# Kernel optimization log

Measured on AMD Instinct MI355X. Metric: run time of the kernel, lower is better.

The kernel has to match this reference:

```python
import jax, jax.numpy as jnp
import numpy as np

N_HEAD = 16


def setup_inputs() -> dict:
    key = jax.random.key(0)
    ks = jax.random.split(key, 5)
    B, T, C = 4, 2048, 1024
    # torch Linear stored as [out,in]; we use [in,out] so x @ W matches x @ W_t.T
    return {
        "x": jax.random.normal(ks[0], (B, T, C), jnp.float32),
        "c_attn_w": jax.random.normal(ks[1], (C, 3 * C), jnp.float32) * 0.02,
        "c_attn_b": jax.random.normal(ks[2], (3 * C,), jnp.float32) * 0.02,
        "c_proj_w": jax.random.normal(ks[3], (C, C), jnp.float32) * 0.02,
        "c_proj_b": jax.random.normal(ks[4], (C,), jnp.float32) * 0.02,
    }


def reference(x, c_attn_w, c_attn_b, c_proj_w, c_proj_b):
    B, T, C = x.shape
    H = N_HEAD
    d = C // H
    qkv = x @ c_attn_w + c_attn_b                      # [B,T,3C]
    q, k, v = jnp.split(qkv, 3, axis=2)
    q = q.reshape(B, T, H, d).transpose(0, 2, 1, 3)    # [B,H,T,d]
    k = k.reshape(B, T, H, d).transpose(0, 2, 1, 3)
    v = v.reshape(B, T, H, d).transpose(0, 2, 1, 3)
    scale = 1.0 / jnp.sqrt(jnp.asarray(d, x.dtype))
    w = jnp.einsum("bhqd,bhkd->bhqk", q, k) * scale    # [B,H,T,T]
    causal = jnp.tril(jnp.ones((T, T), bool))
    w = jnp.where(causal, w, jnp.asarray(-jnp.inf, w.dtype))
    w = jax.nn.softmax(w, axis=-1)
    y = jnp.einsum("bhqk,bhkd->bhqd", w, v)            # [B,H,T,d]
    y = y.transpose(0, 2, 1, 3).reshape(B, T, C)
    return y @ c_proj_w + c_proj_b
```

## Files before the change

kernel.cpp:

```cpp
#include <hip/hip_runtime.h>
#include <hip/hip_bf16.h>
#include <stdint.h>

#define DEV __device__ __forceinline__

typedef __attribute__((ext_vector_type(8))) short short8;
typedef __attribute__((ext_vector_type(8))) _Float16 half8;
typedef __attribute__((ext_vector_type(2))) __fp16 fp16x2;
typedef __attribute__((ext_vector_type(4))) float floatx4;
typedef __attribute__((ext_vector_type(16))) float floatx16;

DEV unsigned short f2bf(float f) {
  union { float f; uint32_t u; } v; v.f = f;
  uint32_t u = v.u;
  u += 0x7fffu + ((u >> 16) & 1u);
  return (unsigned short)(u >> 16);
}
DEV unsigned short f2h(float f) {
  union { _Float16 h; unsigned short u; } c; c.h = (_Float16)f; return c.u;
}
DEV void async_cp16(const unsigned short* g, unsigned short* l) {
  __builtin_amdgcn_global_load_lds(
      (const __attribute__((address_space(1))) uint32_t*)g,
      (__attribute__((address_space(3))) uint32_t*)l, 16, 0, 0);
}

__global__ __launch_bounds__(256)
void cvt_x_kernel(const float* __restrict__ x, unsigned short* __restrict__ xb) {
  const size_t i = ((size_t)blockIdx.x * 256 + threadIdx.x) * 4;
  const float4 f = *(const float4*)(x + i);
  ushort4 w;
  w.x = f2bf(f.x); w.y = f2bf(f.y); w.z = f2bf(f.z); w.w = f2bf(f.w);
  *(ushort4*)(xb + i) = w;
}

__global__ __launch_bounds__(256)
void transpose_w_kernel(const float* __restrict__ W, unsigned short* __restrict__ Wt,
                        int K, int N) {
  __shared__ float tile[64][65];
  const int k0 = blockIdx.y * 64, n0 = blockIdx.x * 64;
  const int tr = threadIdx.x >> 4;
  const int tc = (threadIdx.x & 15) * 4;
#pragma unroll
  for (int it = 0; it < 4; ++it) {
    const int k = tr + it * 16;
    const float4 f = *(const float4*)(W + (size_t)(k0 + k) * N + n0 + tc);
    tile[k][tc + 0] = f.x; tile[k][tc + 1] = f.y;
    tile[k][tc + 2] = f.z; tile[k][tc + 3] = f.w;
  }
  __syncthreads();
#pragma unroll
  for (int it = 0; it < 4; ++it) {
    const int n = tr + it * 16;
    ushort4 w;
    w.x = f2bf(tile[tc + 0][n]); w.y = f2bf(tile[tc + 1][n]);
    w.z = f2bf(tile[tc + 2][n]); w.w = f2bf(tile[tc + 3][n]);
    *(ushort4*)(Wt + (size_t)(n0 + n) * K + k0 + tc) = w;
  }
}

template <int EPI>
__global__ __launch_bounds__(256)
void gemm_bt_kernel(const unsigned short* __restrict__ A,
                    const unsigned short* __restrict__ Bt,
                    const float* __restrict__ bias, int M, int N, int K,
                    unsigned short* __restrict__ qws,
                    unsigned short* __restrict__ kws,
                    unsigned short* __restrict__ vws,
                    float* __restrict__ out) {
  __shared__ __align__(16) unsigned short As[128 * 32];
  __shared__ __align__(16) unsigned short Bs[128 * 32];
  const int tid = threadIdx.x;
  const int wid = tid >> 6, lane = tid & 63;
  const int quad = lane >> 4, l16 = lane & 15;
  const int wm = wid >> 1, wn = wid & 1;
  const int rowA0 = blockIdx.y * 128;
  const int colB0 = blockIdx.x * 128;

  const int srow = wid * 32 + (lane >> 2);
  const int sko = (lane & 3) * 8;
  const unsigned short* gA0 = A + (size_t)(rowA0 + srow) * K + sko;
  const unsigned short* gA1 = A + (size_t)(rowA0 + srow + 16) * K + sko;
  const unsigned short* gB0 = Bt + (size_t)(colB0 + srow) * K + sko;
  const unsigned short* gB1 = Bt + (size_t)(colB0 + srow + 16) * K + sko;
  unsigned short* lA0 = &As[(wid * 128 + 0) * 8];
  unsigned short* lA1 = &As[(wid * 128 + 64) * 8];
  unsigned short* lB0 = &Bs[(wid * 128 + 0) * 8];
  unsigned short* lB1 = &Bs[(wid * 128 + 64) * 8];

  floatx4 acc[4][4];
#pragma unroll
  for (int i = 0; i < 4; ++i)
#pragma unroll
    for (int j = 0; j < 4; ++j) acc[i][j] = (floatx4){0.f, 0.f, 0.f, 0.f};

  for (int kt = 0; kt < K; kt += 32) {
    __syncthreads();
    async_cp16(gA0 + kt, lA0);
    async_cp16(gA1 + kt, lA1);
    async_cp16(gB0 + kt, lB0);
    async_cp16(gB1 + kt, lB1);
    __syncthreads();

    short8 af[4], bfr[4];
#pragma unroll
    for (int i = 0; i < 4; ++i) {
      af[i] = *(const short8*)&As[(wm * 64 + i * 16 + l16) * 32 + quad * 8];
      bfr[i] = *(const short8*)&Bs[(wn * 64 + i * 16 + l16) * 32 + quad * 8];
    }
#pragma unroll
    for (int i = 0; i < 4; ++i)
#pragma unroll
      for (int j = 0; j < 4; ++j)
        acc[i][j] =
            __builtin_amdgcn_mfma_f32_16x16x32_bf16(af[i], bfr[j], acc[i][j], 0, 0, 0);
  }

#pragma unroll
  for (int i = 0; i < 4; ++i) {
#pragma unroll
    for (int j = 0; j < 4; ++j) {
      const int row0 = rowA0 + wm * 64 + i * 16 + quad * 4;
      const int col = colB0 + wn * 64 + j * 16 + l16;
      const float bv = bias[col];
#pragma unroll
      for (int r = 0; r < 4; ++r) {
        const float v = acc[i][j][r] + bv;
        const int R = row0 + r;
        if constexpr (EPI == 0) {
          const int b = R >> 11, t = R & 2047;
          const int which = col >> 10, c = col & 1023;
          const int h = c >> 6, dd = c & 63;
          const size_t bh = (size_t)(b * 16 + h);
          if (which == 0)
            qws[(bh * 2048 + t) * 64 + dd] = f2bf(v * 0.125f);
          else if (which == 1)
            kws[(bh * 2048 + t) * 64 + dd] = f2bf(v);
          else
            vws[(bh * 64 + dd) * 2048 + t] = f2h(v);
        } else {
          out[(size_t)R * N + col] = v;
        }
      }
    }
  }
}

__global__ __launch_bounds__(256, 2)
void attn_mfma_kernel(const unsigned short* __restrict__ qws,
                      const unsigned short* __restrict__ kws,
                      const unsigned short* __restrict__ vws,
                      unsigned short* __restrict__ yws) {
  constexpr int T = 2048, D = 64;
  __shared__ __align__(16) unsigned short Ks[128 * 72];
  __shared__ __align__(16) unsigned short Vs[64 * 136];
  const int tid = threadIdx.x;
  const int wid = tid >> 6, lane = tid & 63;
  const int hf = lane >> 5, l32 = lane & 31;
  const int bh = blockIdx.x;
  const int qt = 15 - (int)blockIdx.y;
  const int qbase = qt * 128;
  const unsigned short* Qp = qws + (size_t)bh * T * D;
  const unsigned short* Kp = kws + (size_t)bh * T * D;
  const unsigned short* Vp = vws + (size_t)bh * D * T;

  const int q = qbase + wid * 32 + l32;
  short8 qf[4];
#pragma unroll
  for (int s = 0; s < 4; ++s)
    qf[s] = *(const short8*)(Qp + (size_t)q * D + s * 16 + hf * 8);

  floatx16 Oacc[2];
#pragma unroll
  for (int mt2 = 0; mt2 < 2; ++mt2)
#pragma unroll
    for (int i = 0; i < 16; ++i) Oacc[mt2][i] = 0.f;
  float mrun = -1e30f, lrun = 0.f;

  for (int kt = 0; kt <= qt; ++kt) {
    const int kb = kt * 128;
    __syncthreads();
#pragma unroll
    for (int it = 0; it < 4; ++it) {
      const int e = it * 256 + tid;
      {
        const int row = e >> 3, c = (e & 7) * 8;
        *(short8*)&Ks[row * 72 + c] =
            *(const short8*)(Kp + (size_t)(kb + row) * D + c);
      }
      {
        const int row = e >> 4, c = (e & 15) * 8;
        *(short8*)&Vs[row * 136 + c] =
            *(const short8*)(Vp + (size_t)row * T + kb + c);
      }
    }
    __syncthreads();

    const bool diag = (kt == qt);
    const int mtmax = diag ? (wid + 1) : 4;

    floatx16 S[4];
#pragma unroll
    for (int mt = 0; mt < 4; ++mt)
      if (mt < mtmax)
#pragma unroll
        for (int i = 0; i < 16; ++i) S[mt][i] = 0.f;

#pragma unroll
    for (int s = 0; s < 4; ++s) {
#pragma unroll
      for (int mt = 0; mt < 4; ++mt)
        if (mt < mtmax) {
          const short8 kf =
              *(const short8*)&Ks[(mt * 32 + l32) * 72 + s * 16 + hf * 8];
          S[mt] = __builtin_amdgcn_mfma_f32_32x32x16_bf16(kf, qf[s], S[mt], 0, 0, 0);
        }
    }

    if (diag) {
#pragma unroll
      for (int mt = 0; mt < 4; ++mt)
        if (mt == wid) {
#pragma unroll
          for (int r = 0; r < 16; ++r) {
            const int intra = (r & 3) + 8 * (r >> 2) + 4 * hf;
            if (intra > l32) S[mt][r] = -1e30f;
          }
        }
    }

    float tmax = -1e30f;
#pragma unroll
    for (int mt = 0; mt < 4; ++mt)
      if (mt < mtmax)
#pragma unroll
        for (int r = 0; r < 16; ++r) tmax = fmaxf(tmax, S[mt][r]);
    tmax = fmaxf(tmax, __shfl_xor(tmax, 32, 64));
    const float mn = fmaxf(mrun, tmax);
    const float alpha = __expf(mrun - mn);
    mrun = mn;

    float tsum = 0.f;
    uint32_t pk[4][8];
#pragma unroll
    for (int mt = 0; mt < 4; ++mt)
      if (mt < mtmax)
#pragma unroll
        for (int t = 0; t < 8; ++t) {
          const float pa = __expf(S[mt][2 * t] - mn);
          const float pb = __expf(S[mt][2 * t + 1] - mn);
          tsum += pa + pb;
          union { fp16x2 h; uint32_t u; } cv;
          cv.h = __builtin_amdgcn_cvt_pkrtz(pa, pb);
          pk[mt][t] = cv.u;
        }
    tsum += __shfl_xor(tsum, 32, 64);
    lrun = lrun * alpha + tsum;
#pragma unroll
    for (int mt2 = 0; mt2 < 2; ++mt2)
#pragma unroll
      for (int i = 0; i < 16; ++i) Oacc[mt2][i] *= alpha;

    const int smax = 2 * mtmax;
#pragma unroll
    for (int s = 0; s < 8; ++s)
      if (s < smax) {
        const int mt = s >> 1;
        const int bo = 4 * (s & 1);
        const uint32_t own0 = hf ? pk[mt][bo + 2] : pk[mt][bo];
        const uint32_t own1 = hf ? pk[mt][bo + 3] : pk[mt][bo + 1];
        const uint32_t sendA = hf ? pk[mt][bo] : pk[mt][bo + 2];
        const uint32_t sendB = hf ? pk[mt][bo + 1] : pk[mt][bo + 3];
        const uint32_t recvA = (uint32_t)__shfl_xor((int)sendA, 32, 64);
        const uint32_t recvB = (uint32_t)__shfl_xor((int)sendB, 32, 64);
        union { uint32_t u[4]; half8 h; } bb;
        bb.u[0] = hf ? recvA : own0;
        bb.u[1] = hf ? recvB : own1;
        bb.u[2] = hf ? own0 : recvA;
        bb.u[3] = hf ? own1 : recvB;
#pragma unroll
        for (int mt2 = 0; mt2 < 2; ++mt2) {
          const half8 vf =
              *(const half8*)&Vs[(mt2 * 32 + l32) * 136 + s * 16 + hf * 8];
          Oacc[mt2] = __builtin_amdgcn_mfma_f32_32x32x16_f16(vf, bb.h, Oacc[mt2], 0, 0, 0);
        }
      }
  }

  const float invl = 1.0f / lrun;
  const int b_ = bh >> 4, h_ = bh & 15;
  unsigned short* yrow = yws + ((size_t)(b_ * 2048 + q)) * 1024 + h_ * 64;
#pragma unroll
  for (int mt2 = 0; mt2 < 2; ++mt2)
#pragma unroll
    for (int t = 0; t < 8; ++t) {
      const int d0 = mt2 * 32 + 2 * (t & 1) + 8 * (t >> 1) + 4 * hf;
      const uint32_t ua = f2bf(Oacc[mt2][2 * t] * invl);
      const uint32_t ub = f2bf(Oacc[mt2][2 * t + 1] * invl);
      *(uint32_t*)&yrow[d0] = ua | (ub << 16);
    }
}

extern "C" void kernel_launch(void* const* d_in, const int* in_sizes, int n_in,
                              void* d_out, int out_size, void* d_ws, size_t ws_size,
                              hipStream_t stream) {
  (void)in_sizes; (void)n_in; (void)out_size;
  const float* x = (const float*)d_in[0];
  const float* attn_w = (const float*)d_in[1];
  const float* attn_b = (const float*)d_in[2];
  const float* proj_w = (const float*)d_in[3];
  const float* proj_b = (const float*)d_in[4];
  float* out = (float*)d_out;

  const size_t NQ = 8388608;
  unsigned short* qws = (unsigned short*)d_ws;
  unsigned short* kws = qws + NQ;
  unsigned short* vws = kws + NQ;
  unsigned short* yws = vws + NQ;
  unsigned short* xb  = yws + NQ;
  unsigned short* wta = xb + NQ;
  unsigned short* wtp = wta + 3072 * 1024;
  if (ws_size < (5 * NQ + 4 * 1024 * 1024) * sizeof(unsigned short)) return;

  cvt_x_kernel<<<dim3(8192), dim3(256), 0, stream>>>(x, xb);
  transpose_w_kernel<<<dim3(48, 16), dim3(256), 0, stream>>>(attn_w, wta, 1024, 3072);
  transpose_w_kernel<<<dim3(16, 16), dim3(256), 0, stream>>>(proj_w, wtp, 1024, 1024);

  gemm_bt_kernel<0><<<dim3(24, 64), dim3(256), 0, stream>>>(
      xb, wta, attn_b, 8192, 3072, 1024, qws, kws, vws, nullptr);
  attn_mfma_kernel<<<dim3(64, 16), dim3(256), 0, stream>>>(qws, kws, vws, yws);
  gemm_bt_kernel<1><<<dim3(8, 64), dim3(256), 0, stream>>>(
      yws, wtp, proj_b, 8192, 1024, 1024, nullptr, nullptr, nullptr, out);
}
```

Measured before the change: 282.9 us.

## Use 32x32 MFMA with swizzled LDS in GEMM, exp2 softmax with lazy rescale

```diff
diff --git a/kernel.cpp b/kernel.cpp
--- a/kernel.cpp
+++ b/kernel.cpp
@@ -7,8 +7,13 @@
 typedef __attribute__((ext_vector_type(8))) short short8;
 typedef __attribute__((ext_vector_type(8))) _Float16 half8;
 typedef __attribute__((ext_vector_type(2))) __fp16 fp16x2;
-typedef __attribute__((ext_vector_type(4))) float floatx4;
 typedef __attribute__((ext_vector_type(16))) float floatx16;
+
+#if __has_builtin(__builtin_amdgcn_exp2f)
+#define EXP2F __builtin_amdgcn_exp2f
+#else
+#define EXP2F exp2f
+#endif
 
 DEV unsigned short f2bf(float f) {
   union { float f; uint32_t u; } v; v.f = f;
@@ -72,13 +77,13 @@
   __shared__ __align__(16) unsigned short Bs[128 * 32];
   const int tid = threadIdx.x;
   const int wid = tid >> 6, lane = tid & 63;
-  const int quad = lane >> 4, l16 = lane & 15;
+  const int l32 = lane & 31, hf = lane >> 5;
   const int wm = wid >> 1, wn = wid & 1;
   const int rowA0 = blockIdx.y * 128;
   const int colB0 = blockIdx.x * 128;
 
   const int srow = wid * 32 + (lane >> 2);
-  const int sko = (lane & 3) * 8;
+  const int sko = (((lane & 3) ^ ((lane >> 3) & 3))) * 8;
   const unsigned short* gA0 = A + (size_t)(rowA0 + srow) * K + sko;
   const unsigned short* gA1 = A + (size_t)(rowA0 + srow + 16) * K + sko;
   const unsigned short* gB0 = Bt + (size_t)(colB0 + srow) * K + sko;
@@ -88,11 +93,23 @@
   unsigned short* lB0 = &Bs[(wid * 128 + 0) * 8];
   unsigned short* lB1 = &Bs[(wid * 128 + 64) * 8];
 
-  floatx4 acc[4][4];
-#pragma unroll
-  for (int i = 0; i < 4; ++i)
-#pragma unroll
-    for (int j = 0; j < 4; ++j) acc[i][j] = (floatx4){0.f, 0.f, 0.f, 0.f};
+  int aoff[2][2], boff[2][2];
+#pragma unroll
+  for (int ti = 0; ti < 2; ++ti)
+#pragma unroll
+    for (int s = 0; s < 2; ++s) {
+      const int chunk = (2 * s + hf) ^ ((l32 >> 1) & 3);
+      aoff[ti][s] = (wm * 64 + ti * 32 + l32) * 32 + chunk * 8;
+      boff[ti][s] = (wn * 64 + ti * 32 + l32) * 32 + chunk * 8;
+    }
+
+  floatx16 acc[2][2];
+#pragma unroll
+  for (int i = 0; i < 2; ++i)
+#pragma unroll
+    for (int j = 0; j < 2; ++j)
+#pragma unroll
+      for (int r = 0; r < 16; ++r) acc[i][j][r] = 0.f;
 
   for (int kt = 0; kt < K; kt += 32) {
     __syncthreads();
@@ -101,39 +118,38 @@
     async_cp16(gB0 + kt, lB0);
     async_cp16(gB1 + kt, lB1);
     __syncthreads();
-
-    short8 af[4], bfr[4];
-#pragma unroll
-    for (int i = 0; i < 4; ++i) {
-      af[i] = *(const short8*)&As[(wm * 64 + i * 16 + l16) * 32 + quad * 8];
-      bfr[i] = *(const short8*)&Bs[(wn * 64 + i * 16 + l16) * 32 + quad * 8];
-    }
-#pragma unroll
-    for (int i = 0; i < 4; ++i)
-#pragma unroll
-      for (int j = 0; j < 4; ++j)
-        acc[i][j] =
-            __builtin_amdgcn_mfma_f32_16x16x32_bf16(af[i], bfr[j], acc[i][j], 0, 0, 0);
-  }
-
-#pragma unroll
-  for (int i = 0; i < 4; ++i) {
-#pragma unroll
-    for (int j = 0; j < 4; ++j) {
-      const int row0 = rowA0 + wm * 64 + i * 16 + quad * 4;
-      const int col = colB0 + wn * 64 + j * 16 + l16;
+#pragma unroll
+    for (int s = 0; s < 2; ++s) {
+      const short8 a0 = *(const short8*)&As[aoff[0][s]];
+      const short8 a1 = *(const short8*)&As[aoff[1][s]];
+      const short8 b0 = *(const short8*)&Bs[boff[0][s]];
+      const short8 b1 = *(const short8*)&Bs[boff[1][s]];
+      acc[0][0] = __builtin_amdgcn_mfma_f32_32x32x16_bf16(a0, b0, acc[0][0], 0, 0, 0);
+      acc[0][1] = __builtin_amdgcn_mfma_f32_32x32x16_bf16(a0, b1, acc[0][1], 0, 0, 0);
+      acc[1][0] = __builtin_amdgcn_mfma_f32_32x32x16_bf16(a1, b0, acc[1][0], 0, 0, 0);
+      acc[1][1] = __builtin_amdgcn_mfma_f32_32x32x16_bf16(a1, b1, acc[1][1], 0, 0, 0);
+    }
+  }
+
+  constexpr float QSCALE = 0.18033688011112042f;
+#pragma unroll
+  for (int mi = 0; mi < 2; ++mi) {
+#pragma unroll
+    for (int nj = 0; nj < 2; ++nj) {
+      const int col = colB0 + wn * 64 + nj * 32 + l32;
       const float bv = bias[col];
 #pragma unroll
-      for (int r = 0; r < 4; ++r) {
-        const float v = acc[i][j][r] + bv;
-        const int R = row0 + r;
+      for (int reg = 0; reg < 16; ++reg) {
+        const int ri = (reg & 3) + 8 * (reg >> 2) + 4 * hf;
+        const int R = rowA0 + wm * 64 + mi * 32 + ri;
+        const float v = acc[mi][nj][reg] + bv;
         if constexpr (EPI == 0) {
           const int b = R >> 11, t = R & 2047;
           const int which = col >> 10, c = col & 1023;
           const int h = c >> 6, dd = c & 63;
           const size_t bh = (size_t)(b * 16 + h);
           if (which == 0)
-            qws[(bh * 2048 + t) * 64 + dd] = f2bf(v * 0.125f);
+            qws[(bh * 2048 + t) * 64 + dd] = f2bf(v * QSCALE);
           else if (which == 1)
             kws[(bh * 2048 + t) * 64 + dd] = f2bf(v);
           else
@@ -237,8 +253,6 @@
         for (int r = 0; r < 16; ++r) tmax = fmaxf(tmax, S[mt][r]);
     tmax = fmaxf(tmax, __shfl_xor(tmax, 32, 64));
     const float mn = fmaxf(mrun, tmax);
-    const float alpha = __expf(mrun - mn);
-    mrun = mn;
 
     float tsum = 0.f;
     uint32_t pk[4][8];
@@ -247,19 +261,26 @@
       if (mt < mtmax)
 #pragma unroll
         for (int t = 0; t < 8; ++t) {
-          const float pa = __expf(S[mt][2 * t] - mn);
-          const float pb = __expf(S[mt][2 * t + 1] - mn);
+          const float pa = EXP2F(S[mt][2 * t] - mn);
+          const float pb = EXP2F(S[mt][2 * t + 1] - mn);
           tsum += pa + pb;
           union { fp16x2 h; uint32_t u; } cv;
           cv.h = __builtin_amdgcn_cvt_pkrtz(pa, pb);
           pk[mt][t] = cv.u;
         }
     tsum += __shfl_xor(tsum, 32, 64);
-    lrun = lrun * alpha + tsum;
-#pragma unroll
-    for (int mt2 = 0; mt2 < 2; ++mt2)
-#pragma unroll
-      for (int i = 0; i < 16; ++i) Oacc[mt2][i] *= alpha;
+
+    if (__ballot(tmax > mrun)) {
+      const float alpha = EXP2F(mrun - mn);
+      lrun = lrun * alpha + tsum;
+      mrun = mn;
+#pragma unroll
+      for (int mt2 = 0; mt2 < 2; ++mt2)
+#pragma unroll
+        for (int i = 0; i < 16; ++i) Oacc[mt2][i] *= alpha;
+    } else {
+      lrun += tsum;
+    }
 
     const int smax = 2 * mtmax;
 #pragma unroll
```

After: 300.4 us. +6.2%, slower.
